# Optimization experiments

Measured on AMD Instinct MI355X. Metric: run time of the kernel, lower is better.

Reference implementation:

```python
import jax, jax.numpy as jnp
import numpy as np

B, N, C, H = 4, 1024, 768, 12
D = C // H  # head dim = 64
SCALE = D ** -0.5


def setup_inputs() -> dict:
    key = jax.random.key(0)
    ks = jax.random.split(key, 13)
    inp = {
        'q': jax.random.normal(ks[0], (N, B, C), jnp.float32),
        'k': jax.random.normal(ks[1], (N, B, C), jnp.float32),
        'v': jax.random.normal(ks[2], (N, B, C), jnp.float32),
        'attn_mask': jax.random.randint(ks[3], (B, N), 0, 2).astype(bool),
        'Wq': jax.random.normal(ks[4], (C, C), jnp.float32) * 0.02,
        'bq': jax.random.normal(ks[5], (C,), jnp.float32) * 0.02,
        'Wk': jax.random.normal(ks[6], (C, C), jnp.float32) * 0.02,
        'bk': jax.random.normal(ks[7], (C,), jnp.float32) * 0.02,
        'Wv': jax.random.normal(ks[8], (C, C), jnp.float32) * 0.02,
        'bv': jax.random.normal(ks[9], (C,), jnp.float32) * 0.02,
        'Wo': jax.random.normal(ks[10], (C, C), jnp.float32) * 0.02,
        'bo': jax.random.normal(ks[11], (C,), jnp.float32) * 0.02,
        'zeta': jnp.ones((1, H, 1, D), jnp.float32),  # orig (1,1,H,1,D); leading 1 dropped by [0]
    }
    return inp


def reference(q, k, v, attn_mask, Wq, bq, Wk, bk, Wv, bv, Wo, bo, zeta):
    # inputs are [N, B, C]; module permutes to [B, N, C]
    q = q.transpose(1, 0, 2)
    k = k.transpose(1, 0, 2)
    v = v.transpose(1, 0, 2)
    b, n_q, c = q.shape
    n_k = k.shape[1]

    def heads(x, W, bias):
        y = x @ W.T + bias                          # [B, N, C]
        return y.reshape(b, -1, H, D).transpose(0, 2, 1, 3)  # [B, H, N, D]

    qh = heads(q, Wq, bq) * zeta
    kh = heads(k, Wk, bk) * zeta
    vh = heads(v, Wv, bv) * zeta

    scores = jnp.einsum('bhqd,bhkd->bhqk', qh, kh)
    mask_add = jnp.where(attn_mask[:, None, None, :], -jnp.inf, 0.0).astype(scores.dtype)
    # torch path: baddbmm(mask, q, k^T) * scale -> (qk + mask) * scale
    attn = jax.nn.softmax((scores + mask_add) * SCALE, axis=-1)

    x = jnp.einsum('bhqk,bhkd->bhqd', attn, vh)
    x = x.transpose(0, 2, 1, 3).reshape(b, n_q, c)  # [B, N_q, C]
    x = x @ Wo.T + bo
    return x.transpose(1, 0, 2)  # back to [N_q, B, C]
```

## Files before the change

kernel.cpp:

```cpp
#include <hip/hip_runtime.h>
#include <cstdint>
#include <cstddef>

typedef unsigned short us;
using short8 = __attribute__((ext_vector_type(8))) short;
using f32x4  = __attribute__((ext_vector_type(4))) float;

union U8 { us u[8]; short8 v; };
union PU { int w[4]; short8 v; };

#define MFMA16(a,b,c) __builtin_amdgcn_mfma_f32_16x16x32_bf16((a),(b),(c),0,0,0)

static __device__ __forceinline__ us f2bf(float f){
  union { float f; unsigned u; } cv; cv.f = f;
  unsigned u = cv.u;
  return (us)((u + 0x7fffu + ((u >> 16) & 1u)) >> 16);
}

static __device__ __forceinline__ int base_of(const int* nbd, int b){
  int s = 0;
#pragma unroll
  for (int i = 0; i < 3; ++i) if (i < b) s += (nbd[i] + 127) & ~127;
  return s;
}

typedef const __attribute__((address_space(1))) void* gp_t;
typedef __attribute__((address_space(3))) void* lp_t;
#define GL16(g,l) __builtin_amdgcn_global_load_lds((gp_t)(g),(lp_t)(l),16,0,0)

__global__ __launch_bounds__(256) void prep_a(
    const float* __restrict__ xq,
    const float* __restrict__ Wq, const float* __restrict__ Wk,
    const float* __restrict__ Wv, const float* __restrict__ Wo,
    const int* __restrict__ mask,
    us* __restrict__ xbq, us* __restrict__ wb, f32x4* __restrict__ zreg,
    int* __restrict__ rank, int* __restrict__ nbd)
{
  const int bid = blockIdx.x, tid = threadIdx.x;
  if (bid < 4){
    const int b = bid, lane = tid & 63, w = tid >> 6;
    __shared__ int wsum[4];
    int m[4], cnt = 0;
#pragma unroll
    for (int j = 0; j < 4; ++j){
      m[j] = mask[b * 1024 + tid * 4 + j] ? 0 : 1;
      cnt += m[j];
    }
    int sc = cnt;
#pragma unroll
    for (int off = 1; off < 64; off <<= 1){
      int t = __shfl_up(sc, off, 64);
      if (lane >= off) sc += t;
    }
    if (lane == 63) wsum[w] = sc;
    __syncthreads();
    int woff = 0;
#pragma unroll
    for (int i = 0; i < 4; ++i) if (i < w) woff += wsum[i];
    const int total = wsum[0] + wsum[1] + wsum[2] + wsum[3];
    int rr = woff + sc - cnt;
#pragma unroll
    for (int j = 0; j < 4; ++j){
      rank[b * 1024 + tid * 4 + j] = m[j] ? rr : -1;
      rr += m[j];
    }
    if (tid == 0) nbd[b] = total;
    return;
  }
  const float* src; us* dst;
  if (bid < 1156){
    unsigned wi = (bid - 4) * 256u + tid;
    unsigned z  = wi / 73728u;
    unsigned rr = wi - z * 73728u;
    const float* W = (z == 0) ? Wq : (z == 1) ? Wk : (z == 2) ? Wv : Wo;
    src = W  + (size_t)rr * 8u;
    dst = wb + (size_t)z * 589824u + rr * 8u;
  } else if (bid < 2692){
    unsigned id = (bid - 1156) * 256u + tid;
    unsigned row = id / 96u, cc = id - row * 96u;
    unsigned bsel = row >> 10, n = row & 1023u;
    src = xq  + (size_t)(n * 4u + bsel) * 768u + cc * 8u;
    dst = xbq + (size_t)row * 768u + cc * 8u;
  } else {
    zreg[(size_t)(bid - 2692) * 256 + tid] = f32x4{};
    return;
  }
  f32x4 a = *(const f32x4*)src;
  f32x4 b = *(const f32x4*)(src + 4);
  U8 o;
#pragma unroll
  for (int j = 0; j < 4; ++j){ o.u[j] = f2bf(a[j]); o.u[4 + j] = f2bf(b[j]); }
  *(short8*)dst = o.v;
}

__global__ __launch_bounds__(256) void prep_b(
    const float* __restrict__ xk, const float* __restrict__ xv,
    const int* __restrict__ rank, const int* __restrict__ nbd,
    us* __restrict__ xbk, us* __restrict__ xbv)
{
  unsigned id = blockIdx.x * 256u + threadIdx.x;
  unsigned z  = id / 393216u;
  unsigned rr = id - z * 393216u;
  unsigned row = rr / 96u, cc = rr - row * 96u;
  unsigned bsel = row >> 10, n = row & 1023u;
  int rk = rank[row];
  if (rk < 0) return;
  int grow = base_of(nbd, (int)bsel) + rk;
  const float* src = ((z == 0) ? xk : xv) + (size_t)(n * 4u + bsel) * 768u + cc * 8u;
  us* dst = ((z == 0) ? xbk : xbv) + (size_t)grow * 768u + cc * 8u;
  f32x4 a = *(const f32x4*)src;
  f32x4 b = *(const f32x4*)(src + 4);
  U8 o;
#pragma unroll
  for (int j = 0; j < 4; ++j){ o.u[j] = f2bf(a[j]); o.u[4 + j] = f2bf(b[j]); }
  *(short8*)dst = o.v;
}

__global__ __launch_bounds__(512, 1) void qkv_gemm8(
    const us* __restrict__ xbq, const us* __restrict__ xbk, const us* __restrict__ xbv,
    const us* __restrict__ wb,
    const float* __restrict__ bq, const float* __restrict__ bk, const float* __restrict__ bv,
    const float* __restrict__ zeta, const int* __restrict__ nbd,
    us* __restrict__ qh, us* __restrict__ kc, us* __restrict__ vtc)
{
  const int z = blockIdx.z;
  int mt, nt;
  if (z == 0){
    const int flat = blockIdx.x + blockIdx.y * 32;
    const int xcd = flat & 7, c = flat >> 3;
    mt = xcd * 4 + (c & 3);
    nt = c >> 2;
  } else {
    const int mtv = (base_of(nbd, 3) + ((nbd[3] + 127) & ~127)) >> 7;
    const int nlive = 6 * mtv;
    const int c = blockIdx.x + blockIdx.y * 32;
    const int xcd = c & 7, j = c >> 3;
    const int qd = nlive >> 3, rm = nlive & 7;
    const int cnt = qd + (xcd < rm ? 1 : 0);
    if (j >= cnt) return;
    const int start = xcd * qd + (xcd < rm ? xcd : rm);
    const int wk = start + j;
    mt = wk / 6;
    nt = wk - mt * 6;
  }
  const us* A  = (z == 0) ? xbq : (z == 1) ? xbk : xbv;
  const us* Bw = wb + (size_t)z * 589824;
  const float* bias = (z == 0) ? bq : (z == 1) ? bk : bv;

  __shared__ __align__(16) us As[2][128 * 64];
  __shared__ __align__(16) us Bs[2][128 * 64];

  const int tid = threadIdx.x, lane = tid & 63, w = tid >> 6;
  const int wr = (w >> 1) * 32, wc = (w & 1) * 64;

  f32x4 acc[2][4] = {};

  auto STAGE = [&](int kt, int buf){
#pragma unroll
    for (int p = 0; p < 2; ++p){
      int chunk = p * 512 + tid;
      int row = chunk >> 3;
      int colb = ((chunk & 7) ^ (row & 7)) * 8;
      GL16(A  + (size_t)(mt * 128 + row) * 768 + kt * 64 + colb,
           As[buf] + (p * 512 + w * 64) * 8);
      GL16(Bw + (size_t)(nt * 128 + row) * 768 + kt * 64 + colb,
           Bs[buf] + (p * 512 + w * 64) * 8);
    }
  };

  STAGE(0, 0);
  STAGE(1, 1);
  for (int kt = 0; kt < 12; ++kt){
    const int cur = kt & 1;
    if (kt < 11) asm volatile("s_waitcnt vmcnt(4)" ::: "memory");
    else         asm volatile("s_waitcnt vmcnt(0)" ::: "memory");
    __builtin_amdgcn_s_barrier();

#pragma unroll
    for (int ks = 0; ks < 2; ++ks){
      short8 af[2], bf4[4];
#pragma unroll
      for (int mf = 0; mf < 2; ++mf){
        int row = wr + mf * 16 + (lane & 15);
        int byte = (row * 128 + ks * 64 + (lane >> 4) * 16) ^ ((row & 7) << 4);
        af[mf] = *(const short8*)((const char*)As[cur] + byte);
      }
#pragma unroll
      for (int nf = 0; nf < 4; ++nf){
        int row = wc + nf * 16 + (lane & 15);
        int byte = (row * 128 + ks * 64 + (lane >> 4) * 16) ^ ((row & 7) << 4);
        bf4[nf] = *(const short8*)((const char*)Bs[cur] + byte);
      }
#pragma unroll
      for (int mf = 0; mf < 2; ++mf)
#pragma unroll
        for (int nf = 0; nf < 4; ++nf)
          acc[mf][nf] = MFMA16(af[mf], bf4[nf], acc[mf][nf]);
    }

    asm volatile("s_waitcnt lgkmcnt(0)" ::: "memory");
    __builtin_amdgcn_s_barrier();
    if (kt < 10) STAGE(kt + 2, cur);
  }

  float bzv[4], zzv[4]; int colv[4];
#pragma unroll
  for (int nf = 0; nf < 4; ++nf){
    colv[nf] = nt * 128 + wc + nf * 16 + (lane & 15);
    bzv[nf] = bias[colv[nf]];
    zzv[nf] = zeta[colv[nf]];
  }

  if (z == 0){
#pragma unroll
    for (int mf = 0; mf < 2; ++mf)
#pragma unroll
      for (int r = 0; r < 4; ++r){
        int row = mt * 128 + wr + mf * 16 + (lane >> 4) * 4 + r;
#pragma unroll
        for (int nf = 0; nf < 4; ++nf)
          qh[(size_t)row * 768 + colv[nf]] = f2bf((acc[mf][nf][r] + bzv[nf]) * zzv[nf]);
      }
  } else {
    const int row0 = mt * 128;
    const int b0 = base_of(nbd, 1), b1 = base_of(nbd, 2), b2 = base_of(nbd, 3);
    const int bsel = (row0 >= b0) + (row0 >= b1) + (row0 >= b2);
    const int base_b = (bsel == 0) ? 0 : (bsel == 1) ? b0 : (bsel == 2) ? b1 : b2;
    const int nb = nbd[bsel];
#pragma unroll
    for (int mf = 0; mf < 2; ++mf)
#pragma unroll
      for (int r = 0; r < 4; ++r){
        int grow = mt * 128 + wr + mf * 16 + (lane >> 4) * 4 + r;
        int row_local = grow - base_b;
        if (row_local >= nb) continue;
        if (z == 1){
#pragma unroll
          for (int nf = 0; nf < 4; ++nf)
            kc[(size_t)grow * 768 + colv[nf]] =
                f2bf((acc[mf][nf][r] + bzv[nf]) * zzv[nf]);
        } else {
#pragma unroll
          for (int nf = 0; nf < 4; ++nf){
            int hh = colv[nf] >> 6, dd = colv[nf] & 63;
            vtc[((size_t)(bsel * 12 + hh) * 64 + dd) * 1024 + row_local] =
                f2bf((acc[mf][nf][r] + bzv[nf]) * zzv[nf]);
          }
        }
      }
  }
}

__global__ __launch_bounds__(256) void attn_fwd7(
    const us* __restrict__ qh, const us* __restrict__ kc,
    const us* __restrict__ vtc, const int* __restrict__ nbd,
    us* __restrict__ ao)
{
  const int flat = blockIdx.x + 16 * blockIdx.y + 192 * blockIdx.z;
  const int xcd = flat & 7, c = flat >> 3;
  const int pair = xcd * 6 + (c >> 4);
  const int qt = c & 15, h = pair % 12, b = pair / 12;
  const int tid = threadIdx.x, lane = tid & 63, w = tid >> 6;

  const int nbv = nbd[b];
  const int base_b = base_of(nbd, b);
  const int nt = (nbv + 63) >> 6;

  __shared__ __align__(16) us Ks[2][64 * 64];
  __shared__ __align__(16) us Vs[2][64 * 64];

  short8 qf[2];
#pragma unroll
  for (int ks = 0; ks < 2; ++ks)
    qf[ks] = *(const short8*)(qh +
              (size_t)(b * 1024 + qt * 64 + w * 16 + (lane & 15)) * 768 +
              h * 64 + ks * 32 + (lane >> 4) * 8);

  short8 kr[2], vr[2];
  auto KVLOAD = [&](int kt){
#pragma unroll
    for (int p = 0; p < 2; ++p){
      int cc = p * 256 + tid, row = cc >> 3, db = (cc & 7) * 8;
      kr[p] = *(const short8*)(kc + (size_t)(base_b + kt * 64 + row) * 768 + h * 64 + db);
      vr[p] = *(const short8*)(vtc + ((size_t)((b * 12 + h) * 64 + row)) * 1024 + kt * 64 + db);
    }
  };
  auto KVWRITE = [&](int buf){
#pragma unroll
    for (int p = 0; p < 2; ++p){
      int cc = p * 256 + tid, row = cc >> 3, db = (cc & 7) * 8;
      int byte = (row * 128 + db * 2) ^ ((row & 7) << 4);
      *(short8*)((char*)Ks[buf] + byte) = kr[p];
      *(short8*)((char*)Vs[buf] + byte) = vr[p];
    }
  };
  KVLOAD(0); KVWRITE(0);
  __syncthreads();

  const int bpbase = (((lane & 16) << 1) | (lane & 15)) << 2;
  const bool hi5 = (lane & 32) != 0;

  float lsum = 0.f;
  f32x4 o[4] = {};
  int cur = 0;
  for (int kt = 0; kt < nt; ++kt){
    if (kt + 1 < nt) KVLOAD(kt + 1);

    f32x4 s[4] = {};
    __builtin_amdgcn_s_setprio(1);
#pragma unroll
    for (int ks = 0; ks < 2; ++ks)
#pragma unroll
      for (int f = 0; f < 4; ++f){
        int row = f * 16 + (lane & 15);
        short8 kf = *(const short8*)((const char*)Ks[cur] +
                    ((row * 128 + ks * 64 + (lane >> 4) * 16) ^ ((row & 7) << 4)));
        s[f] = MFMA16(kf, qf[ks], s[f]);
      }
    __builtin_amdgcn_s_setprio(0);

    float p_[4][4];
#pragma unroll
    for (int f = 0; f < 4; ++f)
#pragma unroll
      for (int r = 0; r < 4; ++r)
        p_[f][r] = __expf(s[f][r] * 0.125f);
    if (kt == nt - 1){
      int kb = kt * 64 + ((lane >> 4) << 2);
#pragma unroll
      for (int f = 0; f < 4; ++f)
#pragma unroll
        for (int r = 0; r < 4; ++r)
          p_[f][r] = (kb + f * 16 + r < nbv) ? p_[f][r] : 0.f;
    }
#pragma unroll
    for (int f = 0; f < 4; ++f)
      lsum += (p_[f][0] + p_[f][1]) + (p_[f][2] + p_[f][3]);

    unsigned pk[4][2];
#pragma unroll
    for (int f = 0; f < 4; ++f){
      pk[f][0] = (unsigned)f2bf(p_[f][0]) | ((unsigned)f2bf(p_[f][1]) << 16);
      pk[f][1] = (unsigned)f2bf(p_[f][2]) | ((unsigned)f2bf(p_[f][3]) << 16);
    }

    PU pa0, pa1;
#pragma unroll
    for (int j = 0; j < 4; ++j){
      int addr = bpbase + ((j & 2) << 5);
      int wsel = j & 1;
      int t0 = __builtin_amdgcn_ds_bpermute(addr, (int)pk[0][wsel]);
      int t1 = __builtin_amdgcn_ds_bpermute(addr, (int)pk[1][wsel]);
      int t2 = __builtin_amdgcn_ds_bpermute(addr, (int)pk[2][wsel]);
      int t3 = __builtin_amdgcn_ds_bpermute(addr, (int)pk[3][wsel]);
      pa0.w[j] = hi5 ? t1 : t0;
      pa1.w[j] = hi5 ? t3 : t2;
    }

    __builtin_amdgcn_s_setprio(1);
#pragma unroll
    for (int df = 0; df < 4; ++df){
      int vrow = df * 16 + (lane & 15);
      short8 vb0 = *(const short8*)((const char*)Vs[cur] +
                   ((vrow * 128 + 0  + (lane >> 4) * 16) ^ ((vrow & 7) << 4)));
      short8 vb1 = *(const short8*)((const char*)Vs[cur] +
                   ((vrow * 128 + 64 + (lane >> 4) * 16) ^ ((vrow & 7) << 4)));
      o[df] = MFMA16(pa0.v, vb0, o[df]);
      o[df] = MFMA16(pa1.v, vb1, o[df]);
    }
    __builtin_amdgcn_s_setprio(0);

    if (kt + 1 < nt) KVWRITE(cur ^ 1);
    __syncthreads();
    cur ^= 1;
  }

  float l = lsum;
  l += __shfl_xor(l, 16, 64);
  l += __shfl_xor(l, 32, 64);
  float linv[4];
#pragma unroll
  for (int r = 0; r < 4; ++r)
    linv[r] = __builtin_amdgcn_rcpf(__shfl(l, (lane >> 4) * 4 + r, 64));

#pragma unroll
  for (int df = 0; df < 4; ++df)
#pragma unroll
    for (int r = 0; r < 4; ++r){
      int qrow = qt * 64 + w * 16 + (lane >> 4) * 4 + r;
      int dcol = df * 16 + (lane & 15);
      ao[(size_t)(b * 1024 + qrow) * 768 + h * 64 + dcol] = f2bf(o[df][r] * linv[r]);
    }
}

__global__ __launch_bounds__(512, 1) void out_gemm8(
    const us* __restrict__ ain, const us* __restrict__ wo,
    const float* __restrict__ bo, float* __restrict__ dout)
{
  __shared__ __align__(16) us As[2][128 * 64];
  __shared__ __align__(16) us Bs[2][128 * 64];

  const int tid = threadIdx.x, lane = tid & 63, w = tid >> 6;
  const int wr = (w >> 1) * 32, wc = (w & 1) * 64;
  const int flat = blockIdx.x + blockIdx.y * 32;
  const int xcd = flat & 7, c = flat >> 3;
  const int mt = xcd * 4 + (c & 3);
  const int nt = c >> 2;

  f32x4 acc[2][4] = {};

  auto STAGE = [&](int kt, int buf){
#pragma unroll
    for (int p = 0; p < 2; ++p){
      int chunk = p * 512 + tid;
      int row = chunk >> 3;
      int colb = ((chunk & 7) ^ (row & 7)) * 8;
      GL16(ain + (size_t)(mt * 128 + row) * 768 + kt * 64 + colb,
           As[buf] + (p * 512 + w * 64) * 8);
      GL16(wo  + (size_t)(nt * 128 + row) * 768 + kt * 64 + colb,
           Bs[buf] + (p * 512 + w * 64) * 8);
    }
  };

  STAGE(0, 0);
  STAGE(1, 1);
  for (int kt = 0; kt < 12; ++kt){
    const int cur = kt & 1;
    if (kt < 11) asm volatile("s_waitcnt vmcnt(4)" ::: "memory");
    else         asm volatile("s_waitcnt vmcnt(0)" ::: "memory");
    __builtin_amdgcn_s_barrier();

#pragma unroll
    for (int ks = 0; ks < 2; ++ks){
      short8 af[2], bf4[4];
#pragma unroll
      for (int mf = 0; mf < 2; ++mf){
        int row = wr + mf * 16 + (lane & 15);
        int byte = (row * 128 + ks * 64 + (lane >> 4) * 16) ^ ((row & 7) << 4);
        af[mf] = *(const short8*)((const char*)As[cur] + byte);
      }
#pragma unroll
      for (int nf = 0; nf < 4; ++nf){
        int row = wc + nf * 16 + (lane & 15);
        int byte = (row * 128 + ks * 64 + (lane >> 4) * 16) ^ ((row & 7) << 4);
        bf4[nf] = *(const short8*)((const char*)Bs[cur] + byte);
      }
#pragma unroll
      for (int mf = 0; mf < 2; ++mf)
#pragma unroll
        for (int nf = 0; nf < 4; ++nf)
          acc[mf][nf] = MFMA16(af[mf], bf4[nf], acc[mf][nf]);
    }

    asm volatile("s_waitcnt lgkmcnt(0)" ::: "memory");
    __builtin_amdgcn_s_barrier();
    if (kt < 10) STAGE(kt + 2, cur);
  }

#pragma unroll
  for (int nf = 0; nf < 4; ++nf){
    int col = nt * 128 + wc + nf * 16 + (lane & 15);
    float bz = bo[col];
#pragma unroll
    for (int mf = 0; mf < 2; ++mf)
#pragma unroll
      for (int r = 0; r < 4; ++r){
        int row = mt * 128 + wr + mf * 16 + (lane >> 4) * 4 + r;
        int n = row & 1023, bsel = row >> 10;
        dout[(size_t)(n * 4 + bsel) * 768 + col] = acc[mf][nf][r] + bz;
      }
  }
}

extern "C" void kernel_launch(void* const* d_in, const int* in_sizes, int n_in,
                              void* d_out, int out_size, void* d_ws, size_t ws_size,
                              hipStream_t stream)
{
  const float* q    = (const float*)d_in[0];
  const float* k    = (const float*)d_in[1];
  const float* v    = (const float*)d_in[2];
  const int*   mask = (const int*)d_in[3];
  const float* Wq   = (const float*)d_in[4];
  const float* bq   = (const float*)d_in[5];
  const float* Wk   = (const float*)d_in[6];
  const float* bk   = (const float*)d_in[7];
  const float* Wv   = (const float*)d_in[8];
  const float* bv   = (const float*)d_in[9];
  const float* Wo   = (const float*)d_in[10];
  const float* bo   = (const float*)d_in[11];
  const float* zeta = (const float*)d_in[12];

  us* xbq = (us*)d_out;
  us* xbk = xbq + 3145728;
  us* xbv = (us*)d_ws;
  us* wb  = xbv + 3145728;
  us* qh  = wb  + 2359296;
  us* kc  = qh  + 3145728;
  us* vtc = kc  + 3145728;
  int* rank = (int*)(vtc + 3145728);
  int* nbd  = rank + 4096;
  us* ao = xbv;

  prep_a<<<4228, 256, 0, stream>>>(q, Wq, Wk, Wv, Wo, mask,
                                   xbq, wb, (f32x4*)vtc, rank, nbd);
  prep_b<<<3072, 256, 0, stream>>>(k, v, rank, nbd, xbk, xbv);
  qkv_gemm8<<<dim3(32, 6, 3), 512, 0, stream>>>(xbq, xbk, xbv, wb, bq, bk, bv,
                                                zeta, nbd, qh, kc, vtc);
  attn_fwd7<<<dim3(16, 12, 4), 256, 0, stream>>>(qh, kc, vtc, nbd, ao);
  out_gemm8<<<dim3(32, 6, 1), 512, 0, stream>>>(ao, wb + 3 * 589824, bo, (float*)d_out);
}
```

Baseline: 68.02 us.

## Merge K/V compaction into prep kernel with per-block rank recompute and fixed batch bases

Folds the separate prep_b launch into the main prep kernel. Each K/V conversion block now recomputes the mask prefix-scan for its batch in shared memory, which removes the dependency on a global rank array from an earlier kernel. Compacted K/V rows are placed at a fixed per-batch base of b*1024 instead of a packed offset. The QKV GEMM maps live tiles to that padded layout, and attention uses b<<10 as the base. This saves one kernel launch and its global round trip, at the cost of a redundant 1024-element scan in every K/V block and a sparser padded buffer layout.

```diff
diff --git a/kernel.cpp b/kernel.cpp
--- a/kernel.cpp
+++ b/kernel.cpp
@@ -17,54 +17,32 @@
   return (us)((u + 0x7fffu + ((u >> 16) & 1u)) >> 16);
 }
 
-static __device__ __forceinline__ int base_of(const int* nbd, int b){
-  int s = 0;
-#pragma unroll
-  for (int i = 0; i < 3; ++i) if (i < b) s += (nbd[i] + 127) & ~127;
-  return s;
-}
-
 typedef const __attribute__((address_space(1))) void* gp_t;
 typedef __attribute__((address_space(3))) void* lp_t;
 #define GL16(g,l) __builtin_amdgcn_global_load_lds((gp_t)(g),(lp_t)(l),16,0,0)
 
-__global__ __launch_bounds__(256) void prep_a(
-    const float* __restrict__ xq,
+__global__ __launch_bounds__(256) void prep(
+    const float* __restrict__ xq, const float* __restrict__ xk, const float* __restrict__ xv,
     const float* __restrict__ Wq, const float* __restrict__ Wk,
     const float* __restrict__ Wv, const float* __restrict__ Wo,
     const int* __restrict__ mask,
-    us* __restrict__ xbq, us* __restrict__ wb, f32x4* __restrict__ zreg,
-    int* __restrict__ rank, int* __restrict__ nbd)
+    us* __restrict__ xbq, us* __restrict__ xbk, us* __restrict__ xbv,
+    us* __restrict__ wb, f32x4* __restrict__ zreg, int* __restrict__ nbd)
 {
   const int bid = blockIdx.x, tid = threadIdx.x;
+  __shared__ int wsum[4];
+  __shared__ short srank[1024];
+
   if (bid < 4){
     const int b = bid, lane = tid & 63, w = tid >> 6;
-    __shared__ int wsum[4];
-    int m[4], cnt = 0;
-#pragma unroll
-    for (int j = 0; j < 4; ++j){
-      m[j] = mask[b * 1024 + tid * 4 + j] ? 0 : 1;
-      cnt += m[j];
-    }
-    int sc = cnt;
-#pragma unroll
-    for (int off = 1; off < 64; off <<= 1){
-      int t = __shfl_up(sc, off, 64);
-      if (lane >= off) sc += t;
-    }
-    if (lane == 63) wsum[w] = sc;
+    int cnt = 0;
+#pragma unroll
+    for (int j = 0; j < 4; ++j) cnt += mask[b * 1024 + tid * 4 + j] ? 0 : 1;
+#pragma unroll
+    for (int off = 1; off < 64; off <<= 1) cnt += __shfl_xor(cnt, off, 64);
+    if (lane == 0) wsum[w] = cnt;
     __syncthreads();
-    int woff = 0;
-#pragma unroll
-    for (int i = 0; i < 4; ++i) if (i < w) woff += wsum[i];
-    const int total = wsum[0] + wsum[1] + wsum[2] + wsum[3];
-    int rr = woff + sc - cnt;
-#pragma unroll
-    for (int j = 0; j < 4; ++j){
-      rank[b * 1024 + tid * 4 + j] = m[j] ? rr : -1;
-      rr += m[j];
-    }
-    if (tid == 0) nbd[b] = total;
+    if (tid == 0) nbd[b] = wsum[0] + wsum[1] + wsum[2] + wsum[3];
     return;
   }
   const float* src; us* dst;
@@ -81,9 +59,45 @@
     unsigned bsel = row >> 10, n = row & 1023u;
     src = xq  + (size_t)(n * 4u + bsel) * 768u + cc * 8u;
     dst = xbq + (size_t)row * 768u + cc * 8u;
-  } else {
+  } else if (bid < 4228){
     zreg[(size_t)(bid - 2692) * 256 + tid] = f32x4{};
     return;
+  } else {
+    unsigned id = (bid - 4228) * 256u + tid;
+    unsigned z  = id / 393216u;
+    unsigned rr = id - z * 393216u;
+    unsigned row = rr / 96u, cc = rr - row * 96u;
+    unsigned bsel = row >> 10, n = row & 1023u;
+
+    const int lane = tid & 63, w = tid >> 6;
+    int m[4], cnt = 0;
+#pragma unroll
+    for (int j = 0; j < 4; ++j){
+      m[j] = mask[bsel * 1024 + tid * 4 + j] ? 0 : 1;
+      cnt += m[j];
+    }
+    int sc = cnt;
+#pragma unroll
+    for (int off = 1; off < 64; off <<= 1){
+      int t = __shfl_up(sc, off, 64);
+      if (lane >= off) sc += t;
+    }
+    if (lane == 63) wsum[w] = sc;
+    __syncthreads();
+    int woff = 0;
+#pragma unroll
+    for (int i = 0; i < 4; ++i) if (i < w) woff += wsum[i];
+    int rr2 = woff + sc - cnt;
+#pragma unroll
+    for (int j = 0; j < 4; ++j){
+      srank[tid * 4 + j] = (short)(m[j] ? rr2 : -1);
+      rr2 += m[j];
+    }
+    __syncthreads();
+    int rk = srank[n];
+    if (rk < 0) return;
+    src = ((z == 0) ? xk : xv) + (size_t)(n * 4u + bsel) * 768u + cc * 8u;
+    dst = ((z == 0) ? xbk : xbv) + (size_t)(bsel * 1024u + rk) * 768u + cc * 8u;
   }
   f32x4 a = *(const f32x4*)src;
   f32x4 b = *(const f32x4*)(src + 4);
@@ -93,30 +107,7 @@
   *(short8*)dst = o.v;
 }
 
-__global__ __launch_bounds__(256) void prep_b(
-    const float* __restrict__ xk, const float* __restrict__ xv,
-    const int* __restrict__ rank, const int* __restrict__ nbd,
-    us* __restrict__ xbk, us* __restrict__ xbv)
-{
-  unsigned id = blockIdx.x * 256u + threadIdx.x;
-  unsigned z  = id / 393216u;
-  unsigned rr = id - z * 393216u;
-  unsigned row = rr / 96u, cc = rr - row * 96u;
-  unsigned bsel = row >> 10, n = row & 1023u;
-  int rk = rank[row];
-  if (rk < 0) return;
-  int grow = base_of(nbd, (int)bsel) + rk;
-  const float* src = ((z == 0) ? xk : xv) + (size_t)(n * 4u + bsel) * 768u + cc * 8u;
-  us* dst = ((z == 0) ? xbk : xbv) + (size_t)grow * 768u + cc * 8u;
-  f32x4 a = *(const f32x4*)src;
-  f32x4 b = *(const f32x4*)(src + 4);
-  U8 o;
-#pragma unroll
-  for (int j = 0; j < 4; ++j){ o.u[j] = f2bf(a[j]); o.u[4 + j] = f2bf(b[j]); }
-  *(short8*)dst = o.v;
-}
-
-__global__ __launch_bounds__(512, 1) void qkv_gemm8(
+__global__ __launch_bounds__(512, 1) void qkv_gemm9(
     const us* __restrict__ xbq, const us* __restrict__ xbk, const us* __restrict__ xbv,
     const us* __restrict__ wb,
     const float* __restrict__ bq, const float* __restrict__ bk, const float* __restrict__ bv,
@@ -131,8 +122,9 @@
     mt = xcd * 4 + (c & 3);
     nt = c >> 2;
   } else {
-    const int mtv = (base_of(nbd, 3) + ((nbd[3] + 127) & ~127)) >> 7;
-    const int nlive = 6 * mtv;
+    const int mtv0 = (nbd[0] + 127) >> 7, mtv1 = (nbd[1] + 127) >> 7;
+    const int mtv2 = (nbd[2] + 127) >> 7, mtv3 = (nbd[3] + 127) >> 7;
+    const int nlive = 6 * (mtv0 + mtv1 + mtv2 + mtv3);
     const int c = blockIdx.x + blockIdx.y * 32;
     const int xcd = c & 7, j = c >> 3;
     const int qd = nlive >> 3, rm = nlive & 7;
@@ -140,8 +132,13 @@
     if (j >= cnt) return;
     const int start = xcd * qd + (xcd < rm ? xcd : rm);
     const int wk = start + j;
-    mt = wk / 6;
-    nt = wk - mt * 6;
+    int mti = wk / 6;
+    nt = wk - mti * 6;
+    int bsel2 = 0, t = mti;
+    if (t >= mtv0){ t -= mtv0; bsel2 = 1;
+      if (t >= mtv1){ t -= mtv1; bsel2 = 2;
+        if (t >= mtv2){ t -= mtv2; bsel2 = 3; } } }
+    mt = bsel2 * 8 + t;
   }
   const us* A  = (z == 0) ? xbq : (z == 1) ? xbk : xbv;
   const us* Bw = wb + (size_t)z * 589824;
@@ -222,10 +219,8 @@
           qh[(size_t)row * 768 + colv[nf]] = f2bf((acc[mf][nf][r] + bzv[nf]) * zzv[nf]);
       }
   } else {
-    const int row0 = mt * 128;
-    const int b0 = base_of(nbd, 1), b1 = base_of(nbd, 2), b2 = base_of(nbd, 3);
-    const int bsel = (row0 >= b0) + (row0 >= b1) + (row0 >= b2);
-    const int base_b = (bsel == 0) ? 0 : (bsel == 1) ? b0 : (bsel == 2) ? b1 : b2;
+    const int bsel = mt >> 3;
+    const int base_b = bsel << 10;
     const int nb = nbd[bsel];
 #pragma unroll
     for (int mf = 0; mf < 2; ++mf)
@@ -263,7 +258,7 @@
   const int tid = threadIdx.x, lane = tid & 63, w = tid >> 6;
 
   const int nbv = nbd[b];
-  const int base_b = base_of(nbd, b);
+  const int base_b = b << 10;
   const int nt = (nbv + 63) >> 6;
 
   __shared__ __align__(16) us Ks[2][64 * 64];
@@ -497,14 +492,12 @@
   us* qh  = wb  + 2359296;
   us* kc  = qh  + 3145728;
   us* vtc = kc  + 3145728;
-  int* rank = (int*)(vtc + 3145728);
-  int* nbd  = rank + 4096;
+  int* nbd = (int*)(vtc + 3145728);
   us* ao = xbv;
 
-  prep_a<<<4228, 256, 0, stream>>>(q, Wq, Wk, Wv, Wo, mask,
-                                   xbq, wb, (f32x4*)vtc, rank, nbd);
-  prep_b<<<3072, 256, 0, stream>>>(k, v, rank, nbd, xbk, xbv);
-  qkv_gemm8<<<dim3(32, 6, 3), 512, 0, stream>>>(xbq, xbk, xbv, wb, bq, bk, bv,
+  prep<<<7300, 256, 0, stream>>>(q, k, v, Wq, Wk, Wv, Wo, mask,
+                                 xbq, xbk, xbv, wb, (f32x4*)vtc, nbd);
+  qkv_gemm9<<<dim3(32, 6, 3), 512, 0, stream>>>(xbq, xbk, xbv, wb, bq, bk, bv,
                                                 zeta, nbd, qh, kc, vtc);
   attn_fwd7<<<dim3(16, 12, 4), 256, 0, stream>>>(qh, kc, vtc, nbd, ao);
   out_gemm8<<<dim3(32, 6, 1), 512, 0, stream>>>(ao, wb + 3 * 589824, bo, (float*)d_out);
```

Result: no change. 66.71 us, median of 2 (-1.9%).
